# Performance work log

Measured on AMD Instinct MI355X. Metric: run time of the kernel, lower is better.

The kernel has to match this reference:

```python
import jax, jax.numpy as jnp
import numpy as np

B, T, C, H = 512, 256, 768, 64
NEG = -1e9  # finite stand-in for -inf; exp(NEG - max) underflows to exactly 0 in fp32


def setup_inputs() -> dict:
    key = jax.random.key(0)
    kx, kq, kk, kv, kp = jax.random.split(key, 5)
    # xavier_uniform bound for a (H, C) torch Linear weight: sqrt(6/(C+H))
    bound = float(np.sqrt(6.0 / (C + H)))
    return {
        "x": jax.random.normal(kx, (B, T, C), dtype=jnp.float32),
        "Wq": jax.random.uniform(kq, (C, H), jnp.float32, -bound, bound),
        "Wk": jax.random.uniform(kk, (C, H), jnp.float32, -bound, bound),
        "Wv": jax.random.uniform(kv, (C, H), jnp.float32, -bound, bound),
        "pad_mask": jax.random.randint(kp, (B, T), 0, 2, dtype=jnp.int32),
    }


def reference(x, Wq, Wk, Wv, pad_mask):
    # Projections (torch Linear without bias: x @ W.T; W stored here pre-transposed as [C,H])
    q = x @ Wq  # [B,T,H]
    k = x @ Wk
    v = x @ Wv
    scores = jnp.einsum("bth,bsh->bts", q, k) / (H ** 0.5)  # [B,T,T]
    causal = jnp.tril(jnp.ones((T, T), dtype=bool))
    # pad_mask.unsqueeze(-1)==0 masks entire query rows i where pad_mask[b,i]==0
    mask = causal[None, :, :] & (pad_mask[:, :, None] != 0)  # [B,T,T]
    weights = jax.nn.softmax(jnp.where(mask, scores, NEG), axis=-1)
    # torch: fully -inf rows -> softmax NaN -> replaced with zeros
    row_valid = mask.any(axis=-1)  # [B,T]
    weights = jnp.where(row_valid[:, :, None], weights, 0.0)
    # dropout is identity in eval mode
    return weights @ v  # [B,T,H]
```

## Files before the change

kernel.cpp:

```cpp
#include <hip/hip_runtime.h>
#include <hip/hip_bf16.h>

typedef unsigned short u16;
typedef unsigned int u32;
typedef __attribute__((ext_vector_type(8))) short short8;
typedef __attribute__((ext_vector_type(4))) float f32x4;
typedef __attribute__((ext_vector_type(4))) u16 u16x4;

static constexpr int Bb = 512, Tt = 256, Cc = 768, Hh = 64;

__device__ __forceinline__ u16 f2bf(float f) {
    __hip_bfloat16 h = __float2bfloat16(f);
    union { __hip_bfloat16 h; u16 u; } v; v.h = h;
    return v.u;
}

__global__ void wt_kernel(const float* __restrict__ Wq, const float* __restrict__ Wk,
                          const float* __restrict__ Wv, u16* __restrict__ Wf) {
    int idx = blockIdx.x * 256 + threadIdx.x;
    int n = idx / Cc, k = idx % Cc;
    const float* W = (n < 64) ? Wq : (n < 128) ? Wk : Wv;
    float val = W[k * Hh + (n & 63)];
    int nt = n >> 4, fr = n & 15;
    int kc = k >> 6, ksub = (k >> 5) & 1, fk = k & 31;
    Wf[kc * 12288 + (ksub * 12 + nt) * 512 + (fr + ((fk >> 3) << 4)) * 8 + (fk & 7)] = f2bf(val);
}

__global__ __launch_bounds__(512, 2) void fused_kernel(
        const float* __restrict__ x, const u16* __restrict__ Wf,
        const int* __restrict__ pad, float* __restrict__ out) {
    __shared__ u16 smem[57344];
    char* smB = (char*)smem;

    const int tid = threadIdx.x;
    const int w = tid >> 6, l = tid & 63;
    const int lrow = l & 15, lgrp = l >> 4;
    const int b = blockIdx.x;
    const int cswz = (lrow & 7) << 4;
    const int tt0 = w, tt1 = 15 - w;

    const float* xg = x + ((size_t)b * Tt + (tid >> 4)) * Cc + (tid & 15) * 4;

    float4 xrA[8], xrB[8];
    short8 wr[3];
    f32x4 acc[2][12];
#pragma unroll
    for (int i = 0; i < 2; ++i)
#pragma unroll
        for (int j = 0; j < 12; ++j) acc[i][j] = (f32x4)0.f;

#define XLOAD(kc_, R_)                                                         \
    _Pragma("unroll")                                                          \
    for (int j = 0; j < 8; ++j)                                                \
        R_[j] = *(const float4*)(xg + (size_t)j * 32 * Cc + (kc_) * 64);

#define XWRITE(R_, nb_)                                                        \
    {                                                                          \
        char* xb_ = smB + (nb_) * 32768;                                       \
        _Pragma("unroll")                                                      \
        for (int j = 0; j < 8; ++j) {                                          \
            int row = j * 32 + (tid >> 4);                                     \
            u16x4 pk;                                                          \
            pk[0] = f2bf(R_[j].x); pk[1] = f2bf(R_[j].y);                      \
            pk[2] = f2bf(R_[j].z); pk[3] = f2bf(R_[j].w);                      \
            *(u16x4*)(xb_ + ((row * 128 + (tid & 15) * 8) ^ ((row & 7) << 4))) = pk; \
        }                                                                      \
    }

#define WLOADR(kc_)                                                            \
    _Pragma("unroll")                                                          \
    for (int p = 0; p < 3; ++p)                                                \
        wr[p] = *(const short8*)(Wf + (size_t)(kc_) * 12288 + (p * 8 + w) * 512 + l * 8);

#define WWRITE(nb_)                                                            \
    {                                                                          \
        u16* wl_ = smem + 32768 + (nb_) * 12288;                               \
        _Pragma("unroll")                                                      \
        for (int p = 0; p < 3; ++p)                                            \
            *(short8*)(wl_ + (p * 8 + w) * 512 + l * 8) = wr[p];               \
    }

#define COMPUTE(cur_)                                                          \
    {                                                                          \
        const char* xb = smB + (cur_) * 32768;                                 \
        const char* wb = smB + 65536 + (cur_) * 24576;                         \
        _Pragma("unroll")                                                      \
        for (int ksub = 0; ksub < 2; ++ksub) {                                 \
            short8 bfr[12], af[2];                                             \
            _Pragma("unroll")                                                  \
            for (int nt = 0; nt < 12; ++nt)                                    \
                bfr[nt] = *(const short8*)(wb + (ksub * 12 + nt) * 1024 + l * 16); \
            af[0] = *(const short8*)(xb +                                      \
                (((tt0 * 16 + lrow) * 128 + ksub * 64 + lgrp * 16) ^ cswz));   \
            af[1] = *(const short8*)(xb +                                      \
                (((tt1 * 16 + lrow) * 128 + ksub * 64 + lgrp * 16) ^ cswz));   \
            _Pragma("unroll")                                                  \
            for (int mrep = 0; mrep < 2; ++mrep)                               \
                _Pragma("unroll")                                              \
                for (int nt = 0; nt < 12; ++nt)                                \
                    acc[mrep][nt] = __builtin_amdgcn_mfma_f32_16x16x32_bf16(   \
                        af[mrep], bfr[nt], acc[mrep][nt], 0, 0, 0);            \
        }                                                                      \
    }

#define LBAR() asm volatile("s_waitcnt lgkmcnt(0)\n\ts_barrier" ::: "memory")

    XLOAD(0, xrA);
    WLOADR(0);
    XLOAD(1, xrB);
    XWRITE(xrA, 0);
    WWRITE(0);
    LBAR();

#pragma unroll 1
    for (int ii = 0; ii < 5; ++ii) {
        const int ke = ii * 2;
        {
            WLOADR(ke + 1);
            XLOAD(ke + 2, xrA);
            COMPUTE(0);
            XWRITE(xrB, 1);
            WWRITE(1);
            LBAR();
        }
        {
            WLOADR(ke + 2);
            XLOAD(ke + 3, xrB);
            COMPUTE(1);
            XWRITE(xrA, 0);
            WWRITE(0);
            LBAR();
        }
    }

    WLOADR(11);
    COMPUTE(0);
    XWRITE(xrB, 1);
    WWRITE(1);
    LBAR();
    COMPUTE(1);
    __syncthreads();
#undef XLOAD
#undef XWRITE
#undef WLOADR
#undef WWRITE
#undef COMPUTE
#undef LBAR

#pragma unroll
    for (int mrep = 0; mrep < 2; ++mrep) {
        const int tt = (mrep == 0) ? tt0 : tt1;
        const int s0 = tt * 16;
#pragma unroll
        for (int nt = 0; nt < 12; ++nt) {
            f32x4 a = acc[mrep][nt];
            if (nt < 4) {
                int h = nt * 16 + lrow;
#pragma unroll
                for (int r = 0; r < 4; ++r) {
                    int row = s0 + lgrp * 4 + r;
                    *(u16*)(smB + 65536 + ((row * 128 + h * 2) ^ ((row & 7) << 4))) = f2bf(a[r]);
                }
            } else if (nt < 8) {
                int h = (nt - 4) * 16 + lrow;
#pragma unroll
                for (int r = 0; r < 4; ++r) {
                    int s = s0 + lgrp * 4 + r;
                    *(u16*)(smB + ((s * 128 + h * 2) ^ ((s & 7) << 4))) = f2bf(a[r]);
                }
            } else {
                int h = (nt - 8) * 16 + lrow;
                int s = s0 + lgrp * 4;
                u16x4 pk;
                pk[0] = f2bf(a[0]); pk[1] = f2bf(a[1]);
                pk[2] = f2bf(a[2]); pk[3] = f2bf(a[3]);
                *(u16x4*)(smB + 32768 + h * 512 + ((s * 2) ^ ((h & 15) << 4))) = pk;
            }
        }
    }
    __syncthreads();

    short8 qfr[2][2];
#pragma unroll
    for (int mt = 0; mt < 2; ++mt) {
        const int tt = (mt == 0) ? tt0 : tt1;
#pragma unroll
        for (int kk = 0; kk < 2; ++kk)
            qfr[mt][kk] = *(const short8*)(smB + 65536 +
                (((tt * 16 + lrow) * 128 + kk * 64 + lgrp * 16) ^ cswz));
    }
    __syncthreads();

    char* pbase = smB + 65536 + w * 2560;
#pragma unroll
    for (int mt = 0; mt < 2; ++mt) {
        const int tt = (mt == 0) ? tt0 : tt1;
        const int i0 = tt * 16;

        f32x4 sreg[16];
#pragma unroll
        for (int t = 0; t < 16; ++t) {
            if (t <= tt) {
                short8 k0 = *(const short8*)(smB +
                    (((t * 16 + lrow) * 128 + lgrp * 16) ^ cswz));
                short8 k1 = *(const short8*)(smB +
                    (((t * 16 + lrow) * 128 + 64 + lgrp * 16) ^ cswz));
                f32x4 s = (f32x4)0.f;
                s = __builtin_amdgcn_mfma_f32_16x16x32_bf16(qfr[mt][0], k0, s, 0, 0, 0);
                s = __builtin_amdgcn_mfma_f32_16x16x32_bf16(qfr[mt][1], k1, s, 0, 0, 0);
                if (t == tt) {
#pragma unroll
                    for (int r = 0; r < 4; ++r) {
                        int i = i0 + lgrp * 4 + r;
                        int sidx = t * 16 + lrow;
                        sreg[t][r] = (sidx <= i) ? s[r] * 0.125f : -1e30f;
                    }
                } else {
#pragma unroll
                    for (int r = 0; r < 4; ++r) sreg[t][r] = s[r] * 0.125f;
                }
            }
        }

        f32x4 mx = (f32x4)(-1e30f);
#pragma unroll
        for (int t = 0; t < 16; ++t)
            if (t <= tt)
#pragma unroll
                for (int r = 0; r < 4; ++r) mx[r] = fmaxf(mx[r], sreg[t][r]);
#pragma unroll
        for (int m = 1; m <= 8; m <<= 1)
#pragma unroll
            for (int r = 0; r < 4; ++r) mx[r] = fmaxf(mx[r], __shfl_xor(mx[r], m, 64));

        f32x4 sm = (f32x4)0.f;
#pragma unroll
        for (int t = 0; t < 16; ++t)
            if (t <= tt)
#pragma unroll
                for (int r = 0; r < 4; ++r) {
                    float p = __expf(sreg[t][r] - mx[r]);
                    sreg[t][r] = p;
                    sm[r] += p;
                }
#pragma unroll
        for (int m = 1; m <= 8; m <<= 1)
#pragma unroll
            for (int r = 0; r < 4; ++r) sm[r] += __shfl_xor(sm[r], m, 64);

        float inv[4];
#pragma unroll
        for (int r = 0; r < 4; ++r) {
            int i = i0 + lgrp * 4 + r;
            inv[r] = (pad[b * Tt + i] != 0) ? (1.0f / sm[r]) : 0.0f;
        }

        f32x4 o[4];
#pragma unroll
        for (int ht = 0; ht < 4; ++ht) o[ht] = (f32x4)0.f;
#pragma unroll
        for (int ks = 0; ks < 8; ++ks) {
            if (2 * ks <= tt) {
                char* pb = pbase + (ks & 1) * 1280;
#pragma unroll
                for (int r = 0; r < 4; ++r) {
                    int prow = lgrp * 4 + r;
                    *(u16*)(pb + prow * 80 + lrow * 2) = f2bf(sreg[2 * ks][r]);
                    u16 pv2 = (2 * ks + 1 <= tt) ? f2bf(sreg[2 * ks + 1][r]) : (u16)0;
                    *(u16*)(pb + prow * 80 + 32 + lrow * 2) = pv2;
                }
                short8 pa = *(const short8*)(pb + lrow * 80 + lgrp * 16);
#pragma unroll
                for (int ht = 0; ht < 4; ++ht) {
                    short8 vfr = *(const short8*)(smB + 32768 + (ht * 16 + lrow) * 512 +
                        ((ks * 64 + lgrp * 16) ^ (lrow << 4)));
                    o[ht] = __builtin_amdgcn_mfma_f32_16x16x32_bf16(pa, vfr, o[ht], 0, 0, 0);
                }
            }
        }

        float* outp = out + ((size_t)b * Tt + i0) * Hh;
#pragma unroll
        for (int r = 0; r < 4; ++r)
#pragma unroll
            for (int ht = 0; ht < 4; ++ht)
                outp[(lgrp * 4 + r) * Hh + ht * 16 + lrow] = o[ht][r] * inv[r];
    }
}

extern "C" void kernel_launch(void* const* d_in, const int* in_sizes, int n_in,
                              void* d_out, int out_size, void* d_ws, size_t ws_size,
                              hipStream_t stream) {
    const float* x  = (const float*)d_in[0];
    const float* Wq = (const float*)d_in[1];
    const float* Wk = (const float*)d_in[2];
    const float* Wv = (const float*)d_in[3];
    const int* pad  = (const int*)d_in[4];
    float* out = (float*)d_out;

    u16* Wf = (u16*)d_ws;

    wt_kernel<<<576, 256, 0, stream>>>(Wq, Wk, Wv, Wf);
    fused_kernel<<<Bb, 512, 0, stream>>>(x, Wf, pad, out);
}
```

Baseline: 126.5 us.

## Load x directly into MFMA A-fragment registers, bypassing LDS staging

Each wave now loads its own x rows from global memory straight into the layout the MFMA A operand expects and converts them to bf16 in registers. This removes the shared-memory write and read for the x tile and shrinks LDS use from 112KB to 96KB. Only the weight tiles remain double-buffered in LDS. Global loads become less coalesced, since each lane reads 32-byte pieces spread across rows, and each wave fetches only its own rows with no sharing between waves.

Measured after the change: 171.6 us. 35.6% more time.

```diff
diff --git a/kernel.cpp b/kernel.cpp
--- a/kernel.cpp
+++ b/kernel.cpp
@@ -29,7 +29,7 @@
 __global__ __launch_bounds__(512, 2) void fused_kernel(
         const float* __restrict__ x, const u16* __restrict__ Wf,
         const int* __restrict__ pad, float* __restrict__ out) {
-    __shared__ u16 smem[57344];
+    __shared__ u16 smem[49152];
     char* smB = (char*)smem;
 
     const int tid = threadIdx.x;
@@ -39,9 +39,11 @@
     const int cswz = (lrow & 7) << 4;
     const int tt0 = w, tt1 = 15 - w;
 
-    const float* xg = x + ((size_t)b * Tt + (tid >> 4)) * Cc + (tid & 15) * 4;
+    const float* xga = x + ((size_t)b * Tt + tt0 * 16 + lrow) * Cc + lgrp * 8;
+    const float* xgb = x + ((size_t)b * Tt + tt1 * 16 + lrow) * Cc + lgrp * 8;
 
     float4 xrA[8], xrB[8];
+    short8 af[2][2];
     short8 wr[3];
     f32x4 acc[2][12];
 #pragma unroll
@@ -49,23 +51,29 @@
 #pragma unroll
         for (int j = 0; j < 12; ++j) acc[i][j] = (f32x4)0.f;
 
-#define XLOAD(kc_, R_)                                                         \
+#define XLOADR(kc_, R_)                                                        \
+    R_[0] = *(const float4*)(xga + (kc_) * 64);                                \
+    R_[1] = *(const float4*)(xga + (kc_) * 64 + 4);                            \
+    R_[2] = *(const float4*)(xga + (kc_) * 64 + 32);                           \
+    R_[3] = *(const float4*)(xga + (kc_) * 64 + 36);                           \
+    R_[4] = *(const float4*)(xgb + (kc_) * 64);                                \
+    R_[5] = *(const float4*)(xgb + (kc_) * 64 + 4);                            \
+    R_[6] = *(const float4*)(xgb + (kc_) * 64 + 32);                           \
+    R_[7] = *(const float4*)(xgb + (kc_) * 64 + 36);
+
+#define AFCONV(R_)                                                             \
     _Pragma("unroll")                                                          \
-    for (int j = 0; j < 8; ++j)                                                \
-        R_[j] = *(const float4*)(xg + (size_t)j * 32 * Cc + (kc_) * 64);
-
-#define XWRITE(R_, nb_)                                                        \
-    {                                                                          \
-        char* xb_ = smB + (nb_) * 32768;                                       \
+    for (int mt = 0; mt < 2; ++mt)                                             \
         _Pragma("unroll")                                                      \
-        for (int j = 0; j < 8; ++j) {                                          \
-            int row = j * 32 + (tid >> 4);                                     \
-            u16x4 pk;                                                          \
-            pk[0] = f2bf(R_[j].x); pk[1] = f2bf(R_[j].y);                      \
-            pk[2] = f2bf(R_[j].z); pk[3] = f2bf(R_[j].w);                      \
-            *(u16x4*)(xb_ + ((row * 128 + (tid & 15) * 8) ^ ((row & 7) << 4))) = pk; \
-        }                                                                      \
-    }
+        for (int kk = 0; kk < 2; ++kk) {                                       \
+            float4 a0 = R_[mt * 4 + kk * 2], a1 = R_[mt * 4 + kk * 2 + 1];     \
+            short8 t;                                                          \
+            t[0] = (short)f2bf(a0.x); t[1] = (short)f2bf(a0.y);                \
+            t[2] = (short)f2bf(a0.z); t[3] = (short)f2bf(a0.w);                \
+            t[4] = (short)f2bf(a1.x); t[5] = (short)f2bf(a1.y);                \
+            t[6] = (short)f2bf(a1.z); t[7] = (short)f2bf(a1.w);                \
+            af[mt][kk] = t;                                                    \
+        }
 
 #define WLOADR(kc_)                                                            \
     _Pragma("unroll")                                                          \
@@ -74,7 +82,7 @@
 
 #define WWRITE(nb_)                                                            \
     {                                                                          \
-        u16* wl_ = smem + 32768 + (nb_) * 12288;                               \
+        u16* wl_ = smem + (nb_) * 12288;                                       \
         _Pragma("unroll")                                                      \
         for (int p = 0; p < 3; ++p)                                            \
             *(short8*)(wl_ + (p * 8 + w) * 512 + l * 8) = wr[p];               \
@@ -82,33 +90,27 @@
 
 #define COMPUTE(cur_)                                                          \
     {                                                                          \
-        const char* xb = smB + (cur_) * 32768;                                 \
-        const char* wb = smB + 65536 + (cur_) * 24576;                         \
+        const char* wb = smB + (cur_) * 24576;                                 \
         _Pragma("unroll")                                                      \
         for (int ksub = 0; ksub < 2; ++ksub) {                                 \
-            short8 bfr[12], af[2];                                             \
+            short8 bfr[12];                                                    \
             _Pragma("unroll")                                                  \
             for (int nt = 0; nt < 12; ++nt)                                    \
                 bfr[nt] = *(const short8*)(wb + (ksub * 12 + nt) * 1024 + l * 16); \
-            af[0] = *(const short8*)(xb +                                      \
-                (((tt0 * 16 + lrow) * 128 + ksub * 64 + lgrp * 16) ^ cswz));   \
-            af[1] = *(const short8*)(xb +                                      \
-                (((tt1 * 16 + lrow) * 128 + ksub * 64 + lgrp * 16) ^ cswz));   \
             _Pragma("unroll")                                                  \
-            for (int mrep = 0; mrep < 2; ++mrep)                               \
+            for (int mt = 0; mt < 2; ++mt)                                     \
                 _Pragma("unroll")                                              \
                 for (int nt = 0; nt < 12; ++nt)                                \
-                    acc[mrep][nt] = __builtin_amdgcn_mfma_f32_16x16x32_bf16(   \
-                        af[mrep], bfr[nt], acc[mrep][nt], 0, 0, 0);            \
+                    acc[mt][nt] = __builtin_amdgcn_mfma_f32_16x16x32_bf16(     \
+                        af[mt][ksub], bfr[nt], acc[mt][nt], 0, 0, 0);          \
         }                                                                      \
     }
 
 #define LBAR() asm volatile("s_waitcnt lgkmcnt(0)\n\ts_barrier" ::: "memory")
 
-    XLOAD(0, xrA);
+    XLOADR(0, xrA);
     WLOADR(0);
-    XLOAD(1, xrB);
-    XWRITE(xrA, 0);
+    XLOADR(1, xrB);
     WWRITE(0);
     LBAR();
 
@@ -117,31 +119,32 @@
         const int ke = ii * 2;
         {
             WLOADR(ke + 1);
-            XLOAD(ke + 2, xrA);
+            AFCONV(xrA);
+            XLOADR(ke + 2, xrA);
             COMPUTE(0);
-            XWRITE(xrB, 1);
             WWRITE(1);
             LBAR();
         }
         {
             WLOADR(ke + 2);
-            XLOAD(ke + 3, xrB);
+            AFCONV(xrB);
+            XLOADR(ke + 3, xrB);
             COMPUTE(1);
-            XWRITE(xrA, 0);
             WWRITE(0);
             LBAR();
         }
     }
 
     WLOADR(11);
+    AFCONV(xrA);
     COMPUTE(0);
-    XWRITE(xrB, 1);
     WWRITE(1);
     LBAR();
+    AFCONV(xrB);
     COMPUTE(1);
     __syncthreads();
-#undef XLOAD
-#undef XWRITE
+#undef XLOADR
+#undef AFCONV
 #undef WLOADR
 #undef WWRITE
 #undef COMPUTE
```
